# Performance work log

Measured on AMD Instinct MI355X. Metric: run time of the kernel, lower is better.

## Reference

```python
import jax, jax.numpy as jnp
import numpy as np

TEMPERATURE = 0.05
CLS_W = 0.2
EPS = 1e-8  # torch cosine_similarity denom clamp

BS, D, NEG_NUM = 1024, 1024, 32


def setup_inputs() -> dict:
    key = jax.random.key(0)
    k1, k2, k3 = jax.random.split(key, 3)
    return {
        "text_embeddings": jax.random.normal(k1, (BS, D), dtype=jnp.float32),
        "text_pos_embeddings": jax.random.normal(k2, (BS, D), dtype=jnp.float32),
        "text_neg_embeddings": jax.random.normal(k3, (BS * NEG_NUM, D), dtype=jnp.float32),
    }


def reference(text_embeddings, text_pos_embeddings, text_neg_embeddings):
    bs, d = text_embeddings.shape
    neg_num = text_neg_embeddings.shape[0] // bs

    # Only the block-diagonal of the full bs x (bs*neg_num) cosine matrix is
    # used by the original module, so compute exactly those pairs.
    neg = text_neg_embeddings.reshape(bs, neg_num, d)  # [bs, n, d]

    q_norm = jnp.maximum(jnp.linalg.norm(text_embeddings, axis=-1), EPS)      # [bs]
    p_norm = jnp.maximum(jnp.linalg.norm(text_pos_embeddings, axis=-1), EPS)  # [bs]
    n_norm = jnp.maximum(jnp.linalg.norm(neg, axis=-1), EPS)                  # [bs, n]

    sim_pos = jnp.sum(text_embeddings * text_pos_embeddings, axis=-1) / (q_norm * p_norm)  # [bs]
    sim_neg = jnp.einsum("bd,bnd->bn", text_embeddings, neg) / (q_norm[:, None] * n_norm)  # [bs, n]

    sim = jnp.concatenate([sim_pos[:, None], sim_neg], axis=1) / TEMPERATURE  # [bs, 1+n]
    # cross-entropy with labels = 0 for every row
    loss = -jnp.mean(jax.nn.log_softmax(sim, axis=-1)[:, 0])
    return loss * CLS_W
```

## Files before the change

### kernel.cpp

```cpp
#include <hip/hip_runtime.h>

#define BS 1024
#define D 1024
#define NEG 32
#define TEMP_INV 20.0f
#define CLS_WEIGHT 0.2f
#define EPS 1e-8f

__global__ __launch_bounds__(1024) void cls_sim_kernel(
    const float* __restrict__ q,
    const float* __restrict__ p,
    const float* __restrict__ neg,
    float* __restrict__ row_loss)
{
    const int b    = blockIdx.x;
    const int tid  = threadIdx.x;
    const int lane = tid & 63;
    const int wave = tid >> 6;

    __shared__ float sim_sh[33];

    const float4* q4 = reinterpret_cast<const float4*>(q + (size_t)b * D);
    float4 qv[4];
    #pragma unroll
    for (int j = 0; j < 4; ++j) qv[j] = q4[lane + j * 64];

    const int v0 = wave;
    const int v1 = wave + 16;
    const bool has2 = (wave == 0);

    const float4* p0 = reinterpret_cast<const float4*>(
        (v0 == 0) ? (p + (size_t)b * D)
                  : (neg + ((size_t)b * NEG + (size_t)(v0 - 1)) * (size_t)D));
    const float4* p1 = reinterpret_cast<const float4*>(
        neg + ((size_t)b * NEG + (size_t)(v1 - 1)) * (size_t)D);
    const float4* p2 = reinterpret_cast<const float4*>(
        neg + ((size_t)b * NEG + 31) * (size_t)D);

    float qn = 0.f;
    float s0 = 0.f, n0 = 0.f, s1 = 0.f, n1 = 0.f, s2 = 0.f, n2 = 0.f;

    #pragma unroll
    for (int j = 0; j < 4; ++j) {
        const int i4 = lane + j * 64;
        const float4 a0 = p0[i4];
        const float4 a1 = p1[i4];
        const float4 qq = qv[j];
        qn += qq.x*qq.x + qq.y*qq.y + qq.z*qq.z + qq.w*qq.w;
        s0 += a0.x*qq.x + a0.y*qq.y + a0.z*qq.z + a0.w*qq.w;
        n0 += a0.x*a0.x + a0.y*a0.y + a0.z*a0.z + a0.w*a0.w;
        s1 += a1.x*qq.x + a1.y*qq.y + a1.z*qq.z + a1.w*qq.w;
        n1 += a1.x*a1.x + a1.y*a1.y + a1.z*a1.z + a1.w*a1.w;
    }
    if (has2) {
        #pragma unroll
        for (int j = 0; j < 4; ++j) {
            const int i4 = lane + j * 64;
            const float4 a2 = p2[i4];
            const float4 qq = qv[j];
            s2 += a2.x*qq.x + a2.y*qq.y + a2.z*qq.z + a2.w*qq.w;
            n2 += a2.x*a2.x + a2.y*a2.y + a2.z*a2.z + a2.w*a2.w;
        }
    }

    #pragma unroll
    for (int off = 32; off > 0; off >>= 1) {
        qn += __shfl_down(qn, off);
        s0 += __shfl_down(s0, off);
        n0 += __shfl_down(n0, off);
        s1 += __shfl_down(s1, off);
        n1 += __shfl_down(n1, off);
    }
    if (has2) {
        #pragma unroll
        for (int off = 32; off > 0; off >>= 1) {
            s2 += __shfl_down(s2, off);
            n2 += __shfl_down(n2, off);
        }
    }

    if (lane == 0) {
        const float q_norm = fmaxf(sqrtf(qn), EPS);
        sim_sh[v0] = (s0 / (q_norm * fmaxf(sqrtf(n0), EPS))) * TEMP_INV;
        sim_sh[v1] = (s1 / (q_norm * fmaxf(sqrtf(n1), EPS))) * TEMP_INV;
        if (has2)
            sim_sh[32] = (s2 / (q_norm * fmaxf(sqrtf(n2), EPS))) * TEMP_INV;
    }
    __syncthreads();

    if (wave == 0) {
        const float x = (lane < 33) ? sim_sh[lane] : -1e30f;
        float m = x;
        #pragma unroll
        for (int off = 32; off > 0; off >>= 1)
            m = fmaxf(m, __shfl_down(m, off));
        m = __shfl(m, 0);
        float e = (lane < 33) ? expf(x - m) : 0.f;
        #pragma unroll
        for (int off = 32; off > 0; off >>= 1)
            e += __shfl_down(e, off);
        if (lane == 0)
            row_loss[b] = (m + logf(e)) - sim_sh[0];
    }
}

__global__ __launch_bounds__(256) void cls_loss_reduce_kernel(
    const float* __restrict__ row_loss, float* __restrict__ out)
{
    const int tid  = threadIdx.x;
    const int lane = tid & 63;
    const int wave = tid >> 6;

    __shared__ float partial[4];

    const float4 v = reinterpret_cast<const float4*>(row_loss)[tid];
    float s = v.x + v.y + v.z + v.w;
    #pragma unroll
    for (int off = 32; off > 0; off >>= 1)
        s += __shfl_down(s, off);
    if (lane == 0) partial[wave] = s;
    __syncthreads();
    if (tid == 0) {
        const float total = partial[0] + partial[1] + partial[2] + partial[3];
        out[0] = total * (CLS_WEIGHT / (float)BS);
    }
}

extern "C" void kernel_launch(void* const* d_in, const int* in_sizes, int n_in,
                              void* d_out, int out_size, void* d_ws, size_t ws_size,
                              hipStream_t stream) {
    const float* q   = (const float*)d_in[0];
    const float* p   = (const float*)d_in[1];
    const float* neg = (const float*)d_in[2];
    float* out      = (float*)d_out;
    float* row_loss = (float*)d_ws;

    cls_sim_kernel<<<BS, 1024, 0, stream>>>(q, p, neg, row_loss);
    cls_loss_reduce_kernel<<<1, 256, 0, stream>>>(row_loss, out);
}
```

Before: 31.44 us.

## Fuse final loss reduction via atomics and use 512-thread blocks with 4 vectors per wave

```diff
diff --git a/kernel.cpp b/kernel.cpp
--- a/kernel.cpp
+++ b/kernel.cpp
@@ -7,11 +7,12 @@
 #define CLS_WEIGHT 0.2f
 #define EPS 1e-8f
 
-__global__ __launch_bounds__(1024) void cls_sim_kernel(
+__global__ __launch_bounds__(512) void cls_contrast_fused_kernel(
     const float* __restrict__ q,
     const float* __restrict__ p,
     const float* __restrict__ neg,
-    float* __restrict__ row_loss)
+    float* __restrict__ acc_ws,
+    float* __restrict__ out)
 {
     const int b    = blockIdx.x;
     const int tid  = threadIdx.x;
@@ -25,66 +26,69 @@
     #pragma unroll
     for (int j = 0; j < 4; ++j) qv[j] = q4[lane + j * 64];
 
-    const int v0 = wave;
-    const int v1 = wave + 16;
-    const bool has2 = (wave == 0);
-
-    const float4* p0 = reinterpret_cast<const float4*>(
-        (v0 == 0) ? (p + (size_t)b * D)
-                  : (neg + ((size_t)b * NEG + (size_t)(v0 - 1)) * (size_t)D));
-    const float4* p1 = reinterpret_cast<const float4*>(
-        neg + ((size_t)b * NEG + (size_t)(v1 - 1)) * (size_t)D);
-    const float4* p2 = reinterpret_cast<const float4*>(
+    const float4* vp[4];
+    #pragma unroll
+    for (int k = 0; k < 4; ++k) {
+        const int v = 4 * wave + k;
+        vp[k] = reinterpret_cast<const float4*>(
+            (v == 0) ? (p + (size_t)b * D)
+                     : (neg + ((size_t)b * NEG + (size_t)(v - 1)) * (size_t)D));
+    }
+    const float4* vp4 = reinterpret_cast<const float4*>(
         neg + ((size_t)b * NEG + 31) * (size_t)D);
+    const bool has5 = (wave == 0);
 
     float qn = 0.f;
-    float s0 = 0.f, n0 = 0.f, s1 = 0.f, n1 = 0.f, s2 = 0.f, n2 = 0.f;
+    float s[4] = {0.f, 0.f, 0.f, 0.f};
+    float n[4] = {0.f, 0.f, 0.f, 0.f};
+    float s4 = 0.f, n4 = 0.f;
 
     #pragma unroll
     for (int j = 0; j < 4; ++j) {
         const int i4 = lane + j * 64;
-        const float4 a0 = p0[i4];
-        const float4 a1 = p1[i4];
         const float4 qq = qv[j];
         qn += qq.x*qq.x + qq.y*qq.y + qq.z*qq.z + qq.w*qq.w;
-        s0 += a0.x*qq.x + a0.y*qq.y + a0.z*qq.z + a0.w*qq.w;
-        n0 += a0.x*a0.x + a0.y*a0.y + a0.z*a0.z + a0.w*a0.w;
-        s1 += a1.x*qq.x + a1.y*qq.y + a1.z*qq.z + a1.w*qq.w;
-        n1 += a1.x*a1.x + a1.y*a1.y + a1.z*a1.z + a1.w*a1.w;
-    }
-    if (has2) {
         #pragma unroll
-        for (int j = 0; j < 4; ++j) {
-            const int i4 = lane + j * 64;
-            const float4 a2 = p2[i4];
-            const float4 qq = qv[j];
-            s2 += a2.x*qq.x + a2.y*qq.y + a2.z*qq.z + a2.w*qq.w;
-            n2 += a2.x*a2.x + a2.y*a2.y + a2.z*a2.z + a2.w*a2.w;
+        for (int k = 0; k < 4; ++k) {
+            const float4 a = vp[k][i4];
+            s[k] += a.x*qq.x + a.y*qq.y + a.z*qq.z + a.w*qq.w;
+            n[k] += a.x*a.x  + a.y*a.y  + a.z*a.z  + a.w*a.w;
+        }
+        if (has5) {
+            const float4 a = vp4[i4];
+            s4 += a.x*qq.x + a.y*qq.y + a.z*qq.z + a.w*qq.w;
+            n4 += a.x*a.x  + a.y*a.y  + a.z*a.z  + a.w*a.w;
         }
     }
 
     #pragma unroll
     for (int off = 32; off > 0; off >>= 1) {
-        qn += __shfl_down(qn, off);
-        s0 += __shfl_down(s0, off);
-        n0 += __shfl_down(n0, off);
-        s1 += __shfl_down(s1, off);
-        n1 += __shfl_down(n1, off);
+        qn   += __shfl_down(qn,   off);
+        s[0] += __shfl_down(s[0], off);
+        n[0] += __shfl_down(n[0], off);
+        s[1] += __shfl_down(s[1], off);
+        n[1] += __shfl_down(n[1], off);
+        s[2] += __shfl_down(s[2], off);
+        n[2] += __shfl_down(n[2], off);
+        s[3] += __shfl_down(s[3], off);
+        n[3] += __shfl_down(n[3], off);
     }
-    if (has2) {
+    if (has5) {
         #pragma unroll
         for (int off = 32; off > 0; off >>= 1) {
-            s2 += __shfl_down(s2, off);
-            n2 += __shfl_down(n2, off);
+            s4 += __shfl_down(s4, off);
+            n4 += __shfl_down(n4, off);
         }
     }
 
     if (lane == 0) {
         const float q_norm = fmaxf(sqrtf(qn), EPS);
-        sim_sh[v0] = (s0 / (q_norm * fmaxf(sqrtf(n0), EPS))) * TEMP_INV;
-        sim_sh[v1] = (s1 / (q_norm * fmaxf(sqrtf(n1), EPS))) * TEMP_INV;
-        if (has2)
-            sim_sh[32] = (s2 / (q_norm * fmaxf(sqrtf(n2), EPS))) * TEMP_INV;
+        #pragma unroll
+        for (int k = 0; k < 4; ++k)
+            sim_sh[4 * wave + k] =
+                (s[k] / (q_norm * fmaxf(sqrtf(n[k]), EPS))) * TEMP_INV;
+        if (has5)
+            sim_sh[32] = (s4 / (q_norm * fmaxf(sqrtf(n4), EPS))) * TEMP_INV;
     }
     __syncthreads();
 
@@ -99,30 +103,19 @@
         #pragma unroll
         for (int off = 32; off > 0; off >>= 1)
             e += __shfl_down(e, off);
-        if (lane == 0)
-            row_loss[b] = (m + logf(e)) - sim_sh[0];
-    }
-}
 
-__global__ __launch_bounds__(256) void cls_loss_reduce_kernel(
-    const float* __restrict__ row_loss, float* __restrict__ out)
-{
-    const int tid  = threadIdx.x;
-    const int lane = tid & 63;
-    const int wave = tid >> 6;
-
-    __shared__ float partial[4];
-
-    const float4 v = reinterpret_cast<const float4*>(row_loss)[tid];
-    float s = v.x + v.y + v.z + v.w;
-    #pragma unroll
-    for (int off = 32; off > 0; off >>= 1)
-        s += __shfl_down(s, off);
-    if (lane == 0) partial[wave] = s;
-    __syncthreads();
-    if (tid == 0) {
-        const float total = partial[0] + partial[1] + partial[2] + partial[3];
-        out[0] = total * (CLS_WEIGHT / (float)BS);
+        if (lane == 0) {
+            const float row_loss = (m + logf(e)) - sim_sh[0];
+            atomicAdd(acc_ws, row_loss);
+            __threadfence();
+            unsigned* counter = reinterpret_cast<unsigned*>(acc_ws + 1);
+            const unsigned old = atomicAdd(counter, 1u);
+            if (old == (unsigned)(BS - 1)) {
+                __threadfence();
+                const float total = atomicAdd(acc_ws, 0.0f);
+                out[0] = total * (CLS_WEIGHT / (float)BS);
+            }
+        }
     }
 }
 
@@ -132,9 +125,10 @@
     const float* q   = (const float*)d_in[0];
     const float* p   = (const float*)d_in[1];
     const float* neg = (const float*)d_in[2];
-    float* out      = (float*)d_out;
-    float* row_loss = (float*)d_ws;
+    float* out = (float*)d_out;
+    float* acc = (float*)d_ws;
 
-    cls_sim_kernel<<<BS, 1024, 0, stream>>>(q, p, neg, row_loss);
-    cls_loss_reduce_kernel<<<1, 256, 0, stream>>>(row_loss, out);
+    hipMemsetAsync(acc, 0, 8, stream);
+
+    cls_contrast_fused_kernel<<<BS, 512, 0, stream>>>(q, p, neg, acc, out);
 }
```

New measurement: 62.34 us. +98.3%, slower.
